# Performance work log

Measured on AMD Instinct MI355X. Metric: run time of the kernel, lower is better.

The kernel has to match this reference:

```python
import jax, jax.numpy as jnp
import numpy as np

DIM = 128
N = 4096


def setup_inputs() -> dict:
    key = jax.random.key(0)
    ks = jax.random.split(key, 12)
    d = DIM
    s = 0.02
    inp = jax.random.normal(ks[0], (N, 2 * d), dtype=jnp.float32)
    # H = myLinear: (2d -> 5d -> 1), tanh after each layer
    Hw1 = jax.random.normal(ks[1], (2 * d, 5 * d), dtype=jnp.float32) * s
    Hb1 = jax.random.normal(ks[2], (5 * d,), dtype=jnp.float32) * s
    Hw2 = jax.random.normal(ks[3], (5 * d, 1), dtype=jnp.float32) * s
    Hb2 = jax.random.normal(ks[4], (1,), dtype=jnp.float32) * s
    # augment_f: (d -> 4d -> 8d -> d*d), tanh after each layer
    Aw1 = jax.random.normal(ks[5], (d, 4 * d), dtype=jnp.float32) * s
    Ab1 = jax.random.normal(ks[6], (4 * d,), dtype=jnp.float32) * s
    Aw2 = jax.random.normal(ks[7], (4 * d, 8 * d), dtype=jnp.float32) * s
    Ab2 = jax.random.normal(ks[8], (8 * d,), dtype=jnp.float32) * s
    Aw3 = jax.random.normal(ks[9], (8 * d, d * d), dtype=jnp.float32) * s
    Ab3 = jax.random.normal(ks[10], (d * d,), dtype=jnp.float32) * s
    u = jax.random.uniform(ks[11], (d,), dtype=jnp.float32, minval=-0.001, maxval=0.001)
    return {"t": 0, "inp": inp, "Hw1": Hw1, "Hb1": Hb1, "Hw2": Hw2, "Hb2": Hb2,
            "Aw1": Aw1, "Ab1": Ab1, "Aw2": Aw2, "Ab2": Ab2, "Aw3": Aw3, "Ab3": Ab3, "u": u}


def reference(t, inp, Hw1, Hb1, Hw2, Hb2, Aw1, Ab1, Aw2, Ab2, Aw3, Ab3, u):
    d = DIM
    n = inp.shape[0]

    def H_scalar(z):  # z: [2d] -> scalar
        h = jnp.tanh(z @ Hw1 + Hb1)
        return jnp.tanh(h @ Hw2 + Hb2)[0]

    # per-sample gradient of scalar H w.r.t. input (== batch_jacobian squeeze)
    g = jax.vmap(jax.grad(H_scalar))(inp)  # [N, 2d]
    dx = g[:, :d]
    dv = -g[:, d:]

    x = inp[:, :d]
    h1 = jnp.tanh(x @ Aw1 + Ab1)            # [N, 4d]
    h2 = jnp.tanh(h1 @ Aw2 + Ab2)           # [N, 8d]
    gq = jnp.tanh(h2 @ Aw3 + Ab3).reshape(n, d, d)  # [N, d, d]
    dv = dv + jnp.einsum("nij,j->ni", gq, u)
    return jnp.concatenate([dx, dv], axis=-1)  # [N, 2d]
```

## Files before the change

kernel.cpp:

```cpp
#include <hip/hip_runtime.h>
#include <hip/hip_bf16.h>
#include <cstdint>


typedef __bf16 bf16_t;
typedef __bf16 bf16x4_t __attribute__((ext_vector_type(4)));
typedef __bf16 bf16x8_t __attribute__((ext_vector_type(8)));
typedef float f32x4_t __attribute__((ext_vector_type(4)));
typedef float f32x16_t __attribute__((ext_vector_type(16)));
typedef int intx4_t __attribute__((ext_vector_type(4)));
typedef int intx8_t __attribute__((ext_vector_type(8)));

#define DIMD 128
#define NROW 4096
#define SMEM_G64 8192
#define SMEM3_BYTES 26624

__device__ __forceinline__ float fast_tanh(float x) {
  float t = __builtin_amdgcn_exp2f(x * 2.8853900817779268f);
  return 1.f - 2.f * __builtin_amdgcn_rcpf(t + 1.f);
}

__device__ __forceinline__ uint8_t to_fp8(float x) {
  return (uint8_t)(__builtin_amdgcn_cvt_pk_fp8_f32(x, x, 0, false) & 0xff);
}

__device__ __forceinline__ void g2l16(const void* gp, void* lp) {
  __builtin_amdgcn_global_load_lds(
      reinterpret_cast<__attribute__((address_space(1))) void*>(
          reinterpret_cast<uintptr_t>(gp)),
      reinterpret_cast<__attribute__((address_space(3))) void*>(
          reinterpret_cast<uintptr_t>(lp)),
      16, 0, 0);
}

template <int EPI>
__device__ __forceinline__ void gemm64_body(char* smem, int bx, int by,
                                            const bf16_t* A, int lda,
                                            const bf16_t* B, int ldb, int K,
                                            const float* bias, void* outp,
                                            int ldo) {
  constexpr int BK = 32;
  bf16_t* As = (bf16_t*)smem;
  bf16_t* Bs = As + 2048;

  const int m0 = bx * 64;
  const int n0 = by * 64;
  const int tid = threadIdx.x;
  const int wave = tid >> 6;
  const int lane = tid & 63;
  const int wm = wave >> 1;
  const int wn = wave & 1;

  const int sr = lane >> 2;
  const int sk = (((lane & 3) ^ ((sr >> 1) & 3)) * 8);
  const int fr = lane & 15;
  const int fk = (((lane >> 4) ^ ((fr >> 1) & 3)) * 8);

  f32x4_t acc[2][2] = {};

  for (int k0 = 0; k0 < K; k0 += BK) {
    if (k0) __syncthreads();
    const int rb = wave * 16;
    g2l16(A + (size_t)(m0 + rb + sr) * lda + (k0 + sk), As + rb * BK);
    g2l16(B + (size_t)(n0 + rb + sr) * ldb + (k0 + sk), Bs + rb * BK);
    __syncthreads();

    bf16x8_t af[2], bb[2];
#pragma unroll
    for (int t = 0; t < 2; ++t) {
      af[t] = *(const bf16x8_t*)(As + (wm * 32 + t * 16 + fr) * BK + fk);
      bb[t] = *(const bf16x8_t*)(Bs + (wn * 32 + t * 16 + fr) * BK + fk);
    }
#pragma unroll
    for (int i = 0; i < 2; ++i)
#pragma unroll
      for (int j = 0; j < 2; ++j)
        acc[i][j] = __builtin_amdgcn_mfma_f32_16x16x32_bf16(af[i], bb[j],
                                                            acc[i][j], 0, 0, 0);
  }

#pragma unroll
  for (int i = 0; i < 2; ++i) {
    const int row = m0 + wm * 32 + i * 16 + (lane >> 4) * 4;
#pragma unroll
    for (int j = 0; j < 2; ++j) {
      const int col = n0 + wn * 32 + j * 16 + fr;
      if constexpr (EPI == 0) {
        bf16_t* O = (bf16_t*)outp;
        const float b = bias[col];
#pragma unroll
        for (int r = 0; r < 4; ++r)
          O[(size_t)(row + r) * ldo + col] = (bf16_t)fast_tanh(acc[i][j][r] + b);
      } else if constexpr (EPI == 1) {
        float* O = (float*)outp;
        const bool dx = (n0 < DIMD);
#pragma unroll
        for (int r = 0; r < 4; ++r) {
          const size_t idx = (size_t)(row + r) * ldo + col;
          if (dx) O[idx] = acc[i][j][r];
          else atomicAdd(&O[idx], -acc[i][j][r]);
        }
      } else {
        uint8_t* O = (uint8_t*)outp;
        const float b = bias[col];
#pragma unroll
        for (int r = 0; r < 4; ++r)
          O[(size_t)(row + r) * ldo + col] =
              to_fp8(64.f * fast_tanh(acc[i][j][r] + b));
      }
    }
  }
}

__device__ __forceinline__ void a3_body(char* smem, int bx, int by,
                                        const uint8_t* A, const uint8_t* B,
                                        float* out, const float* ab3,
                                        const float* uvec) {
  constexpr int BK = 64, K = 1024;
  uint8_t* As = (uint8_t*)smem;
  uint8_t* Bs = As + 16384;
  float* red = (float*)(smem + 24576);
  float* us = red + 256;
  float* a3s = us + 128;

  const int m0 = bx * 256;
  const int n0 = by * 128;
  const int tid = threadIdx.x;
  const int wave = tid >> 6;
  const int lane = tid & 63;

  red[tid] = 0.f;
  if (tid < 128) {
    us[tid] = uvec[tid];
    a3s[tid] = ab3[n0 + tid];
  }

  const int sr = lane >> 2;
  const int sk = ((lane & 3) ^ ((sr >> 1) & 3)) * 16;

  const int rl = lane & 31;
  const int w = (rl >> 1) & 3;
  const int c0 = lane >> 5;
  const int sLo = ((2 * c0) ^ w) * 16;
  const int sHi = ((2 * c0 + 1) ^ w) * 16;

  f32x16_t acc[2][4] = {};

  for (int k0 = 0; k0 < K; k0 += BK) {
    if (k0) __syncthreads();
#pragma unroll
    for (int t = 0; t < 4; ++t) {
      const int rb = t * 64 + wave * 16;
      g2l16(A + (size_t)(m0 + rb + sr) * K + (k0 + sk), As + rb * BK);
    }
#pragma unroll
    for (int t = 0; t < 2; ++t) {
      const int rb = t * 64 + wave * 16;
      g2l16(B + (size_t)(n0 + rb + sr) * K + (k0 + sk), Bs + rb * BK);
    }
    __syncthreads();

    intx8_t af[2], bfr[4];
#pragma unroll
    for (int i = 0; i < 2; ++i) {
      const int ra = (wave * 64 + i * 32 + rl) * BK;
      intx4_t lo = *(const intx4_t*)(As + ra + sLo);
      intx4_t hi = *(const intx4_t*)(As + ra + sHi);
      af[i] = __builtin_shufflevector(lo, hi, 0, 1, 2, 3, 4, 5, 6, 7);
    }
#pragma unroll
    for (int j = 0; j < 4; ++j) {
      const int rb2 = (j * 32 + rl) * BK;
      intx4_t lob = *(const intx4_t*)(Bs + rb2 + sLo);
      intx4_t hib = *(const intx4_t*)(Bs + rb2 + sHi);
      bfr[j] = __builtin_shufflevector(lob, hib, 0, 1, 2, 3, 4, 5, 6, 7);
    }
#pragma unroll
    for (int i = 0; i < 2; ++i)
#pragma unroll
      for (int j = 0; j < 4; ++j)
        acc[i][j] = __builtin_amdgcn_mfma_scale_f32_32x32x64_f8f6f4(
            af[i], bfr[j], acc[i][j], 0, 0, 0, 0x79797979, 0, 0x79797979);
  }

  const int q = lane >> 5;
#pragma unroll
  for (int i = 0; i < 2; ++i) {
    float sums[16];
#pragma unroll
    for (int r = 0; r < 16; ++r) sums[r] = 0.f;
#pragma unroll
    for (int j = 0; j < 4; ++j) {
      const int c = j * 32 + rl;
      const float uu = us[c];
      const float b3 = a3s[c];
#pragma unroll
      for (int r = 0; r < 16; ++r) sums[r] += fast_tanh(acc[i][j][r] + b3) * uu;
    }
#pragma unroll
    for (int d = 1; d < 32; d <<= 1)
#pragma unroll
      for (int r = 0; r < 16; ++r) sums[r] += __shfl_xor(sums[r], d, 64);
    if (rl == 0) {
      const int rowb = wave * 64 + i * 32 + 4 * q;
#pragma unroll
      for (int r = 0; r < 16; ++r)
        atomicAdd(&red[rowb + (r & 3) + 8 * (r >> 2)], sums[r]);
    }
  }
  __syncthreads();
  atomicAdd(&out[(size_t)(m0 + tid) * 256 + 128 + by], red[tid]);
}

__device__ __forceinline__ void tcvt_body(char* smem, const float* in,
                                          bf16_t* out, int R, int C, int bx,
                                          int by) {
  float(*t)[33] = (float(*)[33])smem;
  const int c0 = bx * 32;
  const int r0 = by * 32;
  const int tx = threadIdx.x & 31;
  const int ty = threadIdx.x >> 5;
#pragma unroll
  for (int k = 0; k < 4; ++k)
    t[ty + k * 8][tx] = in[(size_t)(r0 + ty + k * 8) * C + c0 + tx];
  __syncthreads();
#pragma unroll
  for (int k = 0; k < 4; ++k)
    out[(size_t)(c0 + ty + k * 8) * R + r0 + tx] = (bf16_t)t[tx][ty + k * 8];
}

__device__ __forceinline__ void aw3t_body(char* smem, const float* Aw3,
                                          uint8_t* Aw3T8, int b) {
  float(*t)[33] = (float(*)[33])smem;
  const int c0 = (b & 511) * 32;
  const int r0 = (b >> 9) * 32;
  const int tx = threadIdx.x & 31;
  const int ty = threadIdx.x >> 5;
#pragma unroll
  for (int k = 0; k < 4; ++k)
    t[ty + k * 8][tx] = Aw3[(size_t)(r0 + ty + k * 8) * 16384 + c0 + tx];
  __syncthreads();
  const int cl = threadIdx.x >> 3;
  const int j = (threadIdx.x & 7) * 4;
  uchar4 v;
  v.x = to_fp8(64.f * t[j + 0][cl]);
  v.y = to_fp8(64.f * t[j + 1][cl]);
  v.z = to_fp8(64.f * t[j + 2][cl]);
  v.w = to_fp8(64.f * t[j + 3][cl]);
  *(uchar4*)(Aw3T8 + (size_t)(c0 + cl) * 1024 + r0 + j) = v;
}

__device__ __forceinline__ void hgrad_row(int row, const bf16_t* h,
                                          const float* Hw2, const float* Hb2,
                                          bf16_t* wout) {
  const int lane = threadIdx.x & 63;
  float hv[10], wv[10];
  float pre2 = 0.f;
#pragma unroll
  for (int t = 0; t < 10; ++t) {
    const int j = lane + t * 64;
    hv[t] = (float)h[(size_t)row * 640 + j];
    wv[t] = Hw2[j];
    pre2 += hv[t] * wv[t];
  }
#pragma unroll
  for (int d = 1; d < 64; d <<= 1) pre2 += __shfl_xor(pre2, d, 64);
  const float y = fast_tanh(pre2 + Hb2[0]);
  const float s = 1.f - y * y;
#pragma unroll
  for (int t = 0; t < 10; ++t) {
    const int j = lane + t * 64;
    wout[(size_t)row * 640 + j] = (bf16_t)(s * wv[t] * (1.f - hv[t] * hv[t]));
  }
}

__global__ __launch_bounds__(256) void launch0(
    const float* __restrict__ inp, bf16_t* __restrict__ inp_bf,
    const float* __restrict__ Hw1, bf16_t* __restrict__ Hw1T,
    bf16_t* __restrict__ Hw1_bf, const float* __restrict__ Aw1,
    bf16_t* __restrict__ Aw1T, const float* __restrict__ Aw2,
    bf16_t* __restrict__ Aw2T, float* __restrict__ out) {
  __shared__ __align__(16) char smem[4224];
  int b = blockIdx.x;
  if (b < 1024) {
    const int i = b * 256 + threadIdx.x;
    const float4 v = ((const float4*)inp)[i];
    bf16x4_t o = {(bf16_t)v.x, (bf16_t)v.y, (bf16_t)v.z, (bf16_t)v.w};
    ((bf16x4_t*)inp_bf)[i] = o;
  } else if (b < 1184) {
    int s = b - 1024;
    tcvt_body(smem, Hw1, Hw1T, 256, 640, s % 20, s / 20);
  } else if (b < 1248) {
    int s = b - 1184;
    tcvt_body(smem, Aw1, Aw1T, 128, 512, s % 16, s / 16);
  } else if (b < 1760) {
    int s = b - 1248;
    tcvt_body(smem, Aw2, Aw2T, 512, 1024, s % 32, s / 32);
  } else if (b < 1920) {
    const int i = (b - 1760) * 256 + threadIdx.x;
    const float4 v = ((const float4*)Hw1)[i];
    bf16x4_t o = {(bf16_t)v.x, (bf16_t)v.y, (bf16_t)v.z, (bf16_t)v.w};
    ((bf16x4_t*)Hw1_bf)[i] = o;
  } else {
    const int i = (b - 1920) * 256 + threadIdx.x;
    ((float4*)out)[i] = make_float4(0.f, 0.f, 0.f, 0.f);
  }
}

__global__ __launch_bounds__(256) void launch1(
    const bf16_t* __restrict__ inp_bf, const bf16_t* __restrict__ Hw1T,
    const float* __restrict__ Hb1, bf16_t* __restrict__ h_bf,
    const bf16_t* __restrict__ Aw1T, const float* __restrict__ Ab1,
    bf16_t* __restrict__ h1_bf, const float* __restrict__ Aw3,
    uint8_t* __restrict__ Aw3T8) {
  __shared__ __align__(16) char smem[SMEM_G64];
  const int b = blockIdx.x;
  if (b < 640) {
    gemm64_body<0>(smem, b % 64, b / 64, inp_bf, 256, Hw1T, 256, 256, Hb1,
                   h_bf, 640);
  } else if (b < 1152) {
    const int i = b - 640;
    gemm64_body<0>(smem, i % 64, i / 64, inp_bf, 256, Aw1T, 128, 128, Ab1,
                   h1_bf, 512);
  } else {
    aw3t_body(smem, Aw3, Aw3T8, b - 1152);
  }
}

__global__ __launch_bounds__(256) void launch2(
    const bf16_t* __restrict__ h1_bf, const bf16_t* __restrict__ Aw2T,
    const float* __restrict__ Ab2, uint8_t* __restrict__ h2_f8,
    const bf16_t* __restrict__ h_bf, const float* __restrict__ Hw2,
    const float* __restrict__ Hb2, bf16_t* __restrict__ w_bf,
    const float* __restrict__ Aw3, uint8_t* __restrict__ Aw3T8) {
  __shared__ __align__(16) char smem[SMEM_G64];
  const int b = blockIdx.x;
  if (b < 1024) {
    gemm64_body<3>(smem, b % 64, b / 64, h1_bf, 512, Aw2T, 512, 512, Ab2,
                   h2_f8, 1024);
  } else if (b < 2048) {
    const int row = (b - 1024) * 4 + (threadIdx.x >> 6);
    hgrad_row(row, h_bf, Hw2, Hb2, w_bf);
  } else {
    aw3t_body(smem, Aw3, Aw3T8, 8192 + (b - 2048));
  }
}

__global__ __launch_bounds__(256) void launch3(
    const bf16_t* __restrict__ w_bf, const bf16_t* __restrict__ Hw1_bf,
    float* __restrict__ out, const uint8_t* __restrict__ h2_f8,
    const uint8_t* __restrict__ Aw3T8, const float* __restrict__ Ab3,
    const float* __restrict__ uvec) {
  __shared__ __align__(16) char smem[SMEM3_BYTES];
  const int b = blockIdx.x;
  if (b < 256) {
    gemm64_body<1>(smem, b % 64, b / 64, w_bf, 640, Hw1_bf, 640, 640, nullptr,
                   out, 256);
  } else {
    const int i = b - 256;
    a3_body(smem, i & 15, i >> 4, h2_f8, Aw3T8, out, Ab3, uvec);
  }
}

extern "C" void kernel_launch(void* const* d_in, const int* in_sizes, int n_in,
                              void* d_out, int out_size, void* d_ws,
                              size_t ws_size, hipStream_t stream) {
  (void)in_sizes; (void)n_in; (void)out_size; (void)ws_size;
  const float* inp = (const float*)d_in[1];
  const float* Hw1 = (const float*)d_in[2];
  const float* Hb1 = (const float*)d_in[3];
  const float* Hw2 = (const float*)d_in[4];
  const float* Hb2 = (const float*)d_in[5];
  const float* Aw1 = (const float*)d_in[6];
  const float* Ab1 = (const float*)d_in[7];
  const float* Aw2 = (const float*)d_in[8];
  const float* Ab2 = (const float*)d_in[9];
  const float* Aw3 = (const float*)d_in[10];
  const float* Ab3 = (const float*)d_in[11];
  const float* u = (const float*)d_in[12];
  float* out = (float*)d_out;

  char* ws = (char*)d_ws;
  bf16_t* inp_bf = (bf16_t*)ws;   ws += (size_t)NROW * 256 * 2;
  bf16_t* Hw1_bf = (bf16_t*)ws;   ws += (size_t)256 * 640 * 2;
  bf16_t* Hw1T = (bf16_t*)ws;     ws += (size_t)640 * 256 * 2;
  bf16_t* Aw1T = (bf16_t*)ws;     ws += (size_t)512 * 128 * 2;
  bf16_t* Aw2T = (bf16_t*)ws;     ws += (size_t)1024 * 512 * 2;
  uint8_t* Aw3T8 = (uint8_t*)ws;  ws += (size_t)16384 * 1024;
  bf16_t* h_bf = (bf16_t*)ws;     ws += (size_t)NROW * 640 * 2;
  bf16_t* w_bf = (bf16_t*)ws;     ws += (size_t)NROW * 640 * 2;
  bf16_t* h1_bf = (bf16_t*)ws;    ws += (size_t)NROW * 512 * 2;
  uint8_t* h2_f8 = (uint8_t*)ws;  ws += (size_t)NROW * 1024;

  launch0<<<2944, 256, 0, stream>>>(inp, inp_bf, Hw1, Hw1T, Hw1_bf, Aw1, Aw1T,
                                    Aw2, Aw2T, out);
  launch1<<<9344, 256, 0, stream>>>(inp_bf, Hw1T, Hb1, h_bf, Aw1T, Ab1, h1_bf,
                                    Aw3, Aw3T8);
  launch2<<<10240, 256, 0, stream>>>(h1_bf, Aw2T, Ab2, h2_f8, h_bf, Hw2, Hb2,
                                     w_bf, Aw3, Aw3T8);
  launch3<<<2304, 256, 0, stream>>>(w_bf, Hw1_bf, out, h2_f8, Aw3T8, Ab3, u);
}
```

Measured before the change: 244.9 us.

## Double-buffer fp8 Aw3 GEMM with 512-thread blocks and swizzled block order

The fused launch3 kernel now runs 512 threads per block. The big fp8 GEMM over the d*d augment output uses 8 waves in a 2x4 layout, each owning fewer accumulators, and a double-buffered LDS pipeline that prefetches the next K tile while computing the current one. Block indices are remapped so that blocks running at the same time share A/B tiles in cache. The Hamiltonian backward GEMM gets its own 512-thread body to fit the new block size. LDS use roughly doubles, which may limit occupancy, and the pipeline waits with a manual vmcnt plus barrier.

```diff
diff --git a/kernel.cpp b/kernel.cpp
--- a/kernel.cpp
+++ b/kernel.cpp
@@ -14,7 +14,7 @@
 #define DIMD 128
 #define NROW 4096
 #define SMEM_G64 8192
-#define SMEM3_BYTES 26624
+#define SMEM3_BYTES 51200
 
 __device__ __forceinline__ float fast_tanh(float x) {
   float t = __builtin_amdgcn_exp2f(x * 2.8853900817779268f);
@@ -92,15 +92,6 @@
 #pragma unroll
         for (int r = 0; r < 4; ++r)
           O[(size_t)(row + r) * ldo + col] = (bf16_t)fast_tanh(acc[i][j][r] + b);
-      } else if constexpr (EPI == 1) {
-        float* O = (float*)outp;
-        const bool dx = (n0 < DIMD);
-#pragma unroll
-        for (int r = 0; r < 4; ++r) {
-          const size_t idx = (size_t)(row + r) * ldo + col;
-          if (dx) O[idx] = acc[i][j][r];
-          else atomicAdd(&O[idx], -acc[i][j][r]);
-        }
       } else {
         uint8_t* O = (uint8_t*)outp;
         const float b = bias[col];
@@ -113,14 +104,71 @@
   }
 }
 
+__device__ __forceinline__ void hbwd64_body(char* smem, int bx, int by,
+                                            const bf16_t* A, int lda,
+                                            const bf16_t* B, int ldb, int K,
+                                            float* out, int ldo) {
+  constexpr int BK = 32;
+  bf16_t* As = (bf16_t*)smem;
+  bf16_t* Bs = As + 2048;
+
+  const int m0 = bx * 64;
+  const int n0 = by * 64;
+  const int tid = threadIdx.x;
+  const int wave = tid >> 6;
+  const int lane = tid & 63;
+  const int wm = wave >> 2;
+  const int wn = wave & 3;
+
+  const int sr = lane >> 2;
+  const int sk = (((lane & 3) ^ ((sr >> 1) & 3)) * 8);
+  const int fr = lane & 15;
+  const int fk = (((lane >> 4) ^ ((fr >> 1) & 3)) * 8);
+
+  f32x4_t acc[2] = {};
+
+  for (int k0 = 0; k0 < K; k0 += BK) {
+    if (k0) __syncthreads();
+    if (wave < 4) {
+      const int rb = wave * 16;
+      g2l16(A + (size_t)(m0 + rb + sr) * lda + (k0 + sk), As + rb * BK);
+    } else {
+      const int rb = (wave - 4) * 16;
+      g2l16(B + (size_t)(n0 + rb + sr) * ldb + (k0 + sk), Bs + rb * BK);
+    }
+    __syncthreads();
+
+    const bf16x8_t bb = *(const bf16x8_t*)(Bs + (wn * 16 + fr) * BK + fk);
+#pragma unroll
+    for (int t = 0; t < 2; ++t) {
+      const bf16x8_t af =
+          *(const bf16x8_t*)(As + (wm * 32 + t * 16 + fr) * BK + fk);
+      acc[t] = __builtin_amdgcn_mfma_f32_16x16x32_bf16(af, bb, acc[t], 0, 0, 0);
+    }
+  }
+
+  const bool dx = (n0 < DIMD);
+  const int col = n0 + wn * 16 + fr;
+#pragma unroll
+  for (int t = 0; t < 2; ++t) {
+    const int row = m0 + wm * 32 + t * 16 + (lane >> 4) * 4;
+#pragma unroll
+    for (int r = 0; r < 4; ++r) {
+      const size_t idx = (size_t)(row + r) * ldo + col;
+      if (dx) out[idx] = acc[t][r];
+      else atomicAdd(&out[idx], -acc[t][r]);
+    }
+  }
+}
+
 __device__ __forceinline__ void a3_body(char* smem, int bx, int by,
                                         const uint8_t* A, const uint8_t* B,
                                         float* out, const float* ab3,
                                         const float* uvec) {
-  constexpr int BK = 64, K = 1024;
+  constexpr int BK = 64, K = 1024, NT = K / BK;
   uint8_t* As = (uint8_t*)smem;
-  uint8_t* Bs = As + 16384;
-  float* red = (float*)(smem + 24576);
+  uint8_t* Bs = As + 32768;
+  float* red = (float*)(smem + 49152);
   float* us = red + 256;
   float* a3s = us + 128;
 
@@ -129,8 +177,10 @@
   const int tid = threadIdx.x;
   const int wave = tid >> 6;
   const int lane = tid & 63;
-
-  red[tid] = 0.f;
+  const int wm = wave >> 1;
+  const int wn = wave & 1;
+
+  if (tid < 256) red[tid] = 0.f;
   if (tid < 128) {
     us[tid] = uvec[tid];
     a3s[tid] = ab3[n0 + tid];
@@ -145,44 +195,55 @@
   const int sLo = ((2 * c0) ^ w) * 16;
   const int sHi = ((2 * c0 + 1) ^ w) * 16;
 
-  f32x16_t acc[2][4] = {};
-
-  for (int k0 = 0; k0 < K; k0 += BK) {
-    if (k0) __syncthreads();
-#pragma unroll
-    for (int t = 0; t < 4; ++t) {
-      const int rb = t * 64 + wave * 16;
-      g2l16(A + (size_t)(m0 + rb + sr) * K + (k0 + sk), As + rb * BK);
-    }
-#pragma unroll
-    for (int t = 0; t < 2; ++t) {
-      const int rb = t * 64 + wave * 16;
-      g2l16(B + (size_t)(n0 + rb + sr) * K + (k0 + sk), Bs + rb * BK);
-    }
-    __syncthreads();
-
-    intx8_t af[2], bfr[4];
+  f32x16_t acc[2][2] = {};
+
+#define A3_STAGE(buf, k0)                                                     \
+  do {                                                                        \
+    uint8_t* Ad = As + (buf) * 16384;                                         \
+    uint8_t* Bd = Bs + (buf) * 8192;                                          \
+    _Pragma("unroll") for (int t_ = 0; t_ < 2; ++t_) {                        \
+      const int rb_ = wave * 32 + t_ * 16;                                    \
+      g2l16(A + (size_t)(m0 + rb_ + sr) * K + ((k0) + sk), Ad + rb_ * BK);    \
+    }                                                                         \
+    const int rbB_ = wave * 16;                                               \
+    g2l16(B + (size_t)(n0 + rbB_ + sr) * K + ((k0) + sk), Bd + rbB_ * BK);    \
+  } while (0)
+
+  A3_STAGE(0, 0);
+  __syncthreads();
+
+  int cur = 0;
+  for (int t = 0; t < NT; ++t) {
+    if (t + 1 < NT) A3_STAGE(cur ^ 1, (t + 1) * BK);
+    const uint8_t* Ab = As + cur * 16384;
+    const uint8_t* Bb = Bs + cur * 8192;
+
+    intx8_t bfr[2];
+#pragma unroll
+    for (int j = 0; j < 2; ++j) {
+      const int rb2 = (wn * 64 + j * 32 + rl) * BK;
+      intx4_t lob = *(const intx4_t*)(Bb + rb2 + sLo);
+      intx4_t hib = *(const intx4_t*)(Bb + rb2 + sHi);
+      bfr[j] = __builtin_shufflevector(lob, hib, 0, 1, 2, 3, 4, 5, 6, 7);
+    }
 #pragma unroll
     for (int i = 0; i < 2; ++i) {
-      const int ra = (wave * 64 + i * 32 + rl) * BK;
-      intx4_t lo = *(const intx4_t*)(As + ra + sLo);
-      intx4_t hi = *(const intx4_t*)(As + ra + sHi);
-      af[i] = __builtin_shufflevector(lo, hi, 0, 1, 2, 3, 4, 5, 6, 7);
-    }
-#pragma unroll
-    for (int j = 0; j < 4; ++j) {
-      const int rb2 = (j * 32 + rl) * BK;
-      intx4_t lob = *(const intx4_t*)(Bs + rb2 + sLo);
-      intx4_t hib = *(const intx4_t*)(Bs + rb2 + sHi);
-      bfr[j] = __builtin_shufflevector(lob, hib, 0, 1, 2, 3, 4, 5, 6, 7);
-    }
-#pragma unroll
-    for (int i = 0; i < 2; ++i)
-#pragma unroll
-      for (int j = 0; j < 4; ++j)
+      const int ra = (wm * 64 + i * 32 + rl) * BK;
+      intx4_t lo = *(const intx4_t*)(Ab + ra + sLo);
+      intx4_t hi = *(const intx4_t*)(Ab + ra + sHi);
+      intx8_t af = __builtin_shufflevector(lo, hi, 0, 1, 2, 3, 4, 5, 6, 7);
+#pragma unroll
+      for (int j = 0; j < 2; ++j)
         acc[i][j] = __builtin_amdgcn_mfma_scale_f32_32x32x64_f8f6f4(
-            af[i], bfr[j], acc[i][j], 0, 0, 0, 0x79797979, 0, 0x79797979);
-  }
+            af, bfr[j], acc[i][j], 0, 0, 0, 0x79797979, 0, 0x79797979);
+    }
+
+    asm volatile("s_waitcnt vmcnt(0)" ::: "memory");
+    __builtin_amdgcn_s_barrier();
+    asm volatile("" ::: "memory");
+    cur ^= 1;
+  }
+#undef A3_STAGE
 
   const int q = lane >> 5;
 #pragma unroll
@@ -191,8 +252,8 @@
 #pragma unroll
     for (int r = 0; r < 16; ++r) sums[r] = 0.f;
 #pragma unroll
-    for (int j = 0; j < 4; ++j) {
-      const int c = j * 32 + rl;
+    for (int j = 0; j < 2; ++j) {
+      const int c = wn * 64 + j * 32 + rl;
       const float uu = us[c];
       const float b3 = a3s[c];
 #pragma unroll
@@ -203,14 +264,15 @@
 #pragma unroll
       for (int r = 0; r < 16; ++r) sums[r] += __shfl_xor(sums[r], d, 64);
     if (rl == 0) {
-      const int rowb = wave * 64 + i * 32 + 4 * q;
+      const int rowb = wm * 64 + i * 32 + 4 * q;
 #pragma unroll
       for (int r = 0; r < 16; ++r)
         atomicAdd(&red[rowb + (r & 3) + 8 * (r >> 2)], sums[r]);
     }
   }
   __syncthreads();
-  atomicAdd(&out[(size_t)(m0 + tid) * 256 + 128 + by], red[tid]);
+  if (tid < 256)
+    atomicAdd(&out[(size_t)(m0 + tid) * 256 + 128 + by], red[tid]);
 }
 
 __device__ __forceinline__ void tcvt_body(char* smem, const float* in,
@@ -347,7 +409,7 @@
   }
 }
 
-__global__ __launch_bounds__(256) void launch3(
+__global__ __launch_bounds__(512, 4) void launch3(
     const bf16_t* __restrict__ w_bf, const bf16_t* __restrict__ Hw1_bf,
     float* __restrict__ out, const uint8_t* __restrict__ h2_f8,
     const uint8_t* __restrict__ Aw3T8, const float* __restrict__ Ab3,
@@ -355,11 +417,12 @@
   __shared__ __align__(16) char smem[SMEM3_BYTES];
   const int b = blockIdx.x;
   if (b < 256) {
-    gemm64_body<1>(smem, b % 64, b / 64, w_bf, 640, Hw1_bf, 640, 640, nullptr,
-                   out, 256);
+    hbwd64_body(smem, b % 64, b / 64, w_bf, 640, Hw1_bf, 640, 640, out, 256);
   } else {
-    const int i = b - 256;
-    a3_body(smem, i & 15, i >> 4, h2_f8, Aw3T8, out, Ab3, uvec);
+    const int p = b - 256;
+    const int by = (p & 7) * 16 + ((p >> 3) & 15);
+    const int bx = p >> 7;
+    a3_body(smem, bx, by, h2_f8, Aw3T8, out, Ab3, uvec);
   }
 }
 
@@ -399,5 +462,5 @@
                                     Aw3, Aw3T8);
   launch2<<<10240, 256, 0, stream>>>(h1_bf, Aw2T, Ab2, h2_f8, h_bf, Hw2, Hb2,
                                      w_bf, Aw3, Aw3T8);
-  launch3<<<2304, 256, 0, stream>>>(w_bf, Hw1_bf, out, h2_f8, Aw3T8, Ab3, u);
-}
+  launch3<<<2304, 512, 0, stream>>>(w_bf, Hw1_bf, out, h2_f8, Aw3T8, Ab3, u);
+}
```

After: 244.6 us. Within noise of the previous version (-0.1%).
